# Kernel tuning notes

Hardware: AMD Instinct MI355X
Metric: run time of the kernel (lower is better)

Reference implementation:

```python
import jax, jax.numpy as jnp
import numpy as np

SQRT_2_OVER_PI = float(np.sqrt(2.0 / np.pi))
EPS = 1e-5
EPS_VAR = 1e-4
NORM_EPS = 1e-12  # F.normalize default


def _gelu_tanh(x):
    return 0.5 * x * (1.0 + jnp.tanh(SQRT_2_OVER_PI * (x + 0.044715 * x ** 3)))


def setup_inputs() -> dict:
    key = jax.random.key(0)
    k1, k2, k3, k4 = jax.random.split(key, 4)
    B, T, D = 4, 4096, 2048
    x = jax.random.normal(k1, (B, T, D), dtype=jnp.float32)
    ema_mean = 0.1 * jax.random.normal(k2, (D,), dtype=jnp.float32)
    # ensure ema_sq - ema_mean^2 > 0 so variance clamp is realistic
    ema_sq = ema_mean ** 2 + jax.random.uniform(k3, (D,), dtype=jnp.float32, minval=0.5, maxval=1.5)
    ema_out = jax.random.normal(k4, (D,), dtype=jnp.float32)
    return {
        "x": x,
        "ema_mean": ema_mean,
        "ema_sq": ema_sq,
        "ema_out": ema_out,
        "surp_ema": jnp.float32(0.05),
        "log_tau": jnp.float32(np.log(2.0)),
        "log_sigma": jnp.float32(np.log(np.exp(0.3) - 1.0)),
        "log_w_raw": jnp.float32(np.log(np.exp(1.0) - 1.0)),
    }


def reference(x, ema_mean, ema_sq, ema_out, surp_ema, log_tau, log_sigma, log_w_raw):
    # learned scalar transforms (differentiable)
    tau = jnp.exp(log_tau)
    sigma = jax.nn.softplus(log_sigma)
    w = jax.nn.softplus(log_w_raw)

    out = _gelu_tanh(x)  # [B,T,D]

    # --- surprise score: z-score vs EMA stats (all detached in torch) ---
    xd = jax.lax.stop_gradient(x)
    mu = jax.lax.stop_gradient(ema_mean)                     # [D]
    var = jnp.maximum(jax.lax.stop_gradient(ema_sq) - mu ** 2, EPS_VAR)
    std = jnp.sqrt(var)                                      # [D]
    z = (xd - mu) / (std + EPS)                               # [B,T,D]
    mean_absz = jnp.mean(jnp.abs(z), axis=-1)                 # [B,T]

    surp_raw = jnp.tanh(sigma * mean_absz)                    # grad flows only via sigma
    surp_mod = jax.nn.relu(surp_raw - jax.lax.stop_gradient(surp_ema))

    # --- cosine similarity of detached output vs EMA direction ---
    outd = jax.lax.stop_gradient(out)
    out_n = outd / jnp.maximum(jnp.linalg.norm(outd, axis=-1, keepdims=True), NORM_EPS)
    eo = jax.lax.stop_gradient(ema_out)
    ema_n = eo / jnp.maximum(jnp.linalg.norm(eo), NORM_EPS)   # [D]
    cos_sim = jnp.clip(jnp.sum(out_n * ema_n, axis=-1), -1.0, 1.0)  # [B,T]

    gate = jnp.exp(-tau * cos_sim) * (1.0 + w * surp_mod)     # [B,T]
    return out * gate[..., None]
```

## Files before the change

kernel.cpp:

```cpp
#include <hip/hip_runtime.h>
#include <math.h>

#define D 2048
#define NT 256

typedef float floatx4 __attribute__((ext_vector_type(4)));

__global__ __launch_bounds__(NT) void fused_gate_kernel(
    const float* __restrict__ x,
    const float* __restrict__ ema_mean,
    const float* __restrict__ ema_sq,
    const float* __restrict__ ema_out,
    const float* __restrict__ surp_ema,
    const float* __restrict__ log_tau,
    const float* __restrict__ log_sigma,
    const float* __restrict__ log_w_raw,
    float* __restrict__ out) {
  const int row = blockIdx.x;
  const int t = threadIdx.x;
  const float* __restrict__ xr = x + (size_t)row * D;
  float* __restrict__ outr = out + (size_t)row * D;

  const float tau    = __expf(log_tau[0]);
  const float sigma  = log1pf(__expf(log_sigma[0]));
  const float w      = log1pf(__expf(log_w_raw[0]));
  const float surp_e = surp_ema[0];

  const float c1 = -2.0f * 0.7978845608028654f;
  const float c2 = c1 * 0.044715f;

  float o[8];
  float s_absz = 0.f, s_o2 = 0.f, s_dot = 0.f, s_e2 = 0.f;

#pragma unroll
  for (int i = 0; i < 2; ++i) {
    const int v = t + i * NT;
    const floatx4 xv = __builtin_nontemporal_load((const floatx4*)xr + v);
    const floatx4 mv = ((const floatx4*)ema_mean)[v];
    const floatx4 qv = ((const floatx4*)ema_sq)[v];
    const floatx4 ev = ((const floatx4*)ema_out)[v];
#pragma unroll
    for (int j = 0; j < 4; ++j) {
      const float xx = xv[j];
      const float x2 = xx * xx;
      const float u2 = xx * fmaf(c2, x2, c1);
      const float g  = xx * __builtin_amdgcn_rcpf(1.0f + __expf(u2));
      o[i * 4 + j] = g;
      const float mu  = mv[j];
      const float var = fmaxf(fmaf(-mu, mu, qv[j]), 1e-4f);
      const float inv = __builtin_amdgcn_rsqf(var);
      s_absz += fabsf((xx - mu) * inv);
      const float e = ev[j];
      s_o2  = fmaf(g, g, s_o2);
      s_dot = fmaf(g, e, s_dot);
      s_e2  = fmaf(e, e, s_e2);
    }
  }

#pragma unroll
  for (int off = 32; off > 0; off >>= 1) {
    s_absz += __shfl_down(s_absz, off);
    s_o2   += __shfl_down(s_o2, off);
    s_dot  += __shfl_down(s_dot, off);
    s_e2   += __shfl_down(s_e2, off);
  }
  __shared__ float sred[4][4];
  const int wave = t >> 6;
  if ((t & 63) == 0) {
    sred[0][wave] = s_absz;
    sred[1][wave] = s_o2;
    sred[2][wave] = s_dot;
    sred[3][wave] = s_e2;
  }
  __syncthreads();
  const float tot_absz = sred[0][0] + sred[0][1] + sred[0][2] + sred[0][3];
  const float tot_o2   = sred[1][0] + sred[1][1] + sred[1][2] + sred[1][3];
  const float tot_dot  = sred[2][0] + sred[2][1] + sred[2][2] + sred[2][3];
  const float tot_e2   = sred[3][0] + sred[3][1] + sred[3][2] + sred[3][3];

  const float mean_absz = tot_absz * (1.0f / (float)D);
  const float surp_raw  = tanhf(sigma * mean_absz);
  const float surp_mod  = fmaxf(surp_raw - surp_e, 0.0f);
  const float inv_no = __builtin_amdgcn_rsqf(fmaxf(tot_o2, 1e-24f));
  const float inv_ne = __builtin_amdgcn_rsqf(fmaxf(tot_e2, 1e-24f));
  float cs = tot_dot * inv_no * inv_ne;
  cs = fminf(fmaxf(cs, -1.0f), 1.0f);
  const float gate = __expf(-tau * cs) * (1.0f + w * surp_mod);

#pragma unroll
  for (int i = 0; i < 2; ++i) {
    const int v = t + i * NT;
    floatx4 r;
    r[0] = o[i * 4 + 0] * gate;
    r[1] = o[i * 4 + 1] * gate;
    r[2] = o[i * 4 + 2] * gate;
    r[3] = o[i * 4 + 3] * gate;
    __builtin_nontemporal_store(r, (floatx4*)outr + v);
  }
}

extern "C" void kernel_launch(void* const* d_in, const int* in_sizes, int n_in,
                              void* d_out, int out_size, void* d_ws, size_t ws_size,
                              hipStream_t stream) {
  const float* x        = (const float*)d_in[0];
  const float* ema_mean = (const float*)d_in[1];
  const float* ema_sq   = (const float*)d_in[2];
  const float* ema_out  = (const float*)d_in[3];
  const float* surp_ema = (const float*)d_in[4];
  const float* log_tau  = (const float*)d_in[5];
  const float* log_sig  = (const float*)d_in[6];
  const float* log_wr   = (const float*)d_in[7];
  float* out = (float*)d_out;

  const int rows = in_sizes[0] / D;

  fused_gate_kernel<<<rows, NT, 0, stream>>>(
      x, ema_mean, ema_sq, ema_out, surp_ema, log_tau, log_sig, log_wr, out);
}
```

Measured before the change: 244.7 us.

## Assign one row per wavefront to remove block-level reduction and barrier

```diff
diff --git a/kernel.cpp b/kernel.cpp
--- a/kernel.cpp
+++ b/kernel.cpp
@@ -3,6 +3,8 @@
 
 #define D 2048
 #define NT 256
+#define ROWS_PER_BLOCK 4
+#define V_PER_LANE 8
 
 typedef float floatx4 __attribute__((ext_vector_type(4)));
 
@@ -16,8 +18,11 @@
     const float* __restrict__ log_sigma,
     const float* __restrict__ log_w_raw,
     float* __restrict__ out) {
-  const int row = blockIdx.x;
   const int t = threadIdx.x;
+  const int lane = t & 63;
+  const int wave = t >> 6;
+  const int row = blockIdx.x * ROWS_PER_BLOCK + wave;
+
   const float* __restrict__ xr = x + (size_t)row * D;
   float* __restrict__ outr = out + (size_t)row * D;
 
@@ -29,12 +34,12 @@
   const float c1 = -2.0f * 0.7978845608028654f;
   const float c2 = c1 * 0.044715f;
 
-  float o[8];
+  float o[V_PER_LANE * 4];
   float s_absz = 0.f, s_o2 = 0.f, s_dot = 0.f, s_e2 = 0.f;
 
 #pragma unroll
-  for (int i = 0; i < 2; ++i) {
-    const int v = t + i * NT;
+  for (int i = 0; i < V_PER_LANE; ++i) {
+    const int v = lane + i * 64;
     const floatx4 xv = __builtin_nontemporal_load((const floatx4*)xr + v);
     const floatx4 mv = ((const floatx4*)ema_mean)[v];
     const floatx4 qv = ((const floatx4*)ema_sq)[v];
@@ -59,37 +64,24 @@
 
 #pragma unroll
   for (int off = 32; off > 0; off >>= 1) {
-    s_absz += __shfl_down(s_absz, off);
-    s_o2   += __shfl_down(s_o2, off);
-    s_dot  += __shfl_down(s_dot, off);
-    s_e2   += __shfl_down(s_e2, off);
+    s_absz += __shfl_xor(s_absz, off);
+    s_o2   += __shfl_xor(s_o2, off);
+    s_dot  += __shfl_xor(s_dot, off);
+    s_e2   += __shfl_xor(s_e2, off);
   }
-  __shared__ float sred[4][4];
-  const int wave = t >> 6;
-  if ((t & 63) == 0) {
-    sred[0][wave] = s_absz;
-    sred[1][wave] = s_o2;
-    sred[2][wave] = s_dot;
-    sred[3][wave] = s_e2;
-  }
-  __syncthreads();
-  const float tot_absz = sred[0][0] + sred[0][1] + sred[0][2] + sred[0][3];
-  const float tot_o2   = sred[1][0] + sred[1][1] + sred[1][2] + sred[1][3];
-  const float tot_dot  = sred[2][0] + sred[2][1] + sred[2][2] + sred[2][3];
-  const float tot_e2   = sred[3][0] + sred[3][1] + sred[3][2] + sred[3][3];
 
-  const float mean_absz = tot_absz * (1.0f / (float)D);
+  const float mean_absz = s_absz * (1.0f / (float)D);
   const float surp_raw  = tanhf(sigma * mean_absz);
   const float surp_mod  = fmaxf(surp_raw - surp_e, 0.0f);
-  const float inv_no = __builtin_amdgcn_rsqf(fmaxf(tot_o2, 1e-24f));
-  const float inv_ne = __builtin_amdgcn_rsqf(fmaxf(tot_e2, 1e-24f));
-  float cs = tot_dot * inv_no * inv_ne;
+  const float inv_no = __builtin_amdgcn_rsqf(fmaxf(s_o2, 1e-24f));
+  const float inv_ne = __builtin_amdgcn_rsqf(fmaxf(s_e2, 1e-24f));
+  float cs = s_dot * inv_no * inv_ne;
   cs = fminf(fmaxf(cs, -1.0f), 1.0f);
   const float gate = __expf(-tau * cs) * (1.0f + w * surp_mod);
 
 #pragma unroll
-  for (int i = 0; i < 2; ++i) {
-    const int v = t + i * NT;
+  for (int i = 0; i < V_PER_LANE; ++i) {
+    const int v = lane + i * 64;
     floatx4 r;
     r[0] = o[i * 4 + 0] * gate;
     r[1] = o[i * 4 + 1] * gate;
@@ -113,7 +105,6 @@
   float* out = (float*)d_out;
 
   const int rows = in_sizes[0] / D;
-
-  fused_gate_kernel<<<rows, NT, 0, stream>>>(
+  fused_gate_kernel<<<rows / ROWS_PER_BLOCK, NT, 0, stream>>>(
       x, ema_mean, ema_sq, ema_out, surp_ema, log_tau, log_sig, log_wr, out);
 }
```

New measurement: 244.6 us. About the same (-0.0%).
